# Kernel optimization log

Measured on AMD Instinct MI355X. Metric: run time of the kernel, lower is better.

Reference implementation:

```python
import jax, jax.numpy as jnp
from jax import lax
import numpy as np

R_ICO = 6          # resolution exponent r
CIN, COUT = 64, 64
RIN, ROUT = 6, 6
CHARTS = 5
H, W = 2 ** R_ICO, 2 ** (R_ICO + 1)
BATCH = 4


def _build_reorder_idx(r, R):
    H_, W_ = 2 ** r, 2 ** (r + 1)
    p = 2 ** r
    idx_in = np.arange(R * 5 * H_ * W_, dtype=np.int64).reshape(R, 5, H_, W_)
    out = np.zeros((R, 5, H_ + 2, W_ + 2), dtype=np.int64)
    out[..., 1:-1, 1:-1] = idx_in
    out[..., 0, 1:p + 1] = np.roll(idx_in, 1, -3)[..., -1, p:]
    out[..., 0, p + 1:-1] = np.roll(np.roll(idx_in, 1, -3), -1, -4)[..., :, -1][..., ::-1]
    out[..., -1, 2:p + 2] = np.roll(np.roll(idx_in, -1, -3), -1, -4)[..., :, 0][..., ::-1]
    out[..., -1, p + 1:-1] = np.roll(idx_in, -1, -3)[..., 0, 0:p]
    out[..., 1:-1, 0] = np.roll(np.roll(idx_in, 1, -3), 1, -4)[..., -1, 0:p][..., ::-1]
    out[..., 2:, -1] = np.roll(np.roll(idx_in, -1, -3), 1, -4)[..., 0, p:][..., ::-1]
    return out


_REORDER = jnp.asarray(_build_reorder_idx(R_ICO, RIN))

# 'baseline' hexagonal kernel index table (idx_k2 == idx_k for baseline)
_IDX_K = np.array([
    [5, 4, -1, 6, 0, 3, -1, 1, 2],
    [4, 3, -1, 5, 0, 2, -1, 6, 1],
    [3, 2, -1, 4, 0, 1, -1, 5, 6],
    [2, 1, -1, 3, 0, 6, -1, 4, 5],
    [1, 6, -1, 2, 0, 5, -1, 3, 4],
    [6, 5, -1, 1, 0, 4, -1, 2, 3]], dtype=np.int64) % 7
# per-output-rotation roll of the Rin axis: idx_r = arange(Rin) rolled i times
_RIN_MAP = np.stack([np.roll(np.arange(RIN), i) for i in range(ROUT)])  # (Rout, Rin)
_MASK3 = np.ones((3, 3), dtype=np.float32)
_MASK3[0, 2] = 0.0  # ret[..., 0, 2] = 0
_MASK3[2, 0] = 0.0  # ret[..., 2, 0] = 0

# CleanVertices: zero the two pole vertices of each chart
_VMASK = np.ones((H, W), dtype=np.float32)
_VMASK[0, -1] = 0.0
_VMASK[-1, 0] = 0.0


def _expand_kernel(weight):
    # weight: (Cout, Cin, Rin, 7)
    # K[co, ci, i, rj, k] = weight[co, ci, rin_map[i, rj], idx_k[i, k]]
    K = weight[:, :, _RIN_MAP[:, :, None], _IDX_K[:, None, :]]  # (Cout, Cin, Rout, Rin, 9)
    K = K.transpose(0, 2, 1, 3, 4).reshape(COUT, ROUT, CIN, RIN, 3, 3)
    K = K * _MASK3  # zero hex-grid corner taps
    # kernel_type='baseline' => idx_k2 == idx_k, so 0.5*K + 0.5*K2 == K
    return K.reshape(COUT * ROUT, CIN * RIN, 3, 3)


def setup_inputs() -> dict:
    key = jax.random.key(0)
    kx, kw = jax.random.split(key)
    s = float(np.sqrt(2.0 / (3 * 3 * CIN * RIN)))
    x = jax.random.normal(kx, (BATCH, CIN, RIN, CHARTS, H, W), dtype=jnp.float32)
    weight = s * jax.random.normal(kw, (COUT, CIN, RIN, 7), dtype=jnp.float32)
    bias = jnp.zeros((COUT,), dtype=jnp.float32)
    return {"x": x, "weight": weight, "bias": bias}


def reference(x, weight, bias):
    B = x.shape[0]
    # CleanVertices on input (inside PadIco.process_vertices)
    x = x * _VMASK
    # icosahedral gather padding: [B, C, R, 5, H, W] -> [B, C, R, 5, H+2, W+2]
    xf = x.reshape(B, CIN, -1)
    xp = jnp.take(xf, _REORDER, axis=-1)
    # fold (C R) -> channels and (charts, H+2) -> height
    ximg = xp.reshape(B, CIN * RIN, CHARTS * (H + 2), W + 2)
    kernel = _expand_kernel(weight)
    y = lax.conv_general_dilated(ximg, kernel, (1, 1), ((1, 1), (1, 1)),
                                 dimension_numbers=('NCHW', 'OIHW', 'NCHW'))
    y = y + jnp.repeat(bias, ROUT)[None, :, None, None]
    y = y.reshape(B, COUT, ROUT, CHARTS, H + 2, W + 2)[..., 1:-1, 1:-1]
    # CleanVertices on output
    return y * _VMASK
```

## Files before the change

kernel.cpp:

```cpp
#include <hip/hip_runtime.h>
#include <hip/hip_bf16.h>

#define BB    4
#define CIN_  64
#define RIN_  6
#define CH_   5
#define HH    64
#define WW_   128
#define KD    384
#define MD    384
#define PH    66
#define PW    130
#define PSZ   (PH*PW)

#define NTAP 7
#define WEXP2_ELEMS (NTAP*MD*KD)
#define WEXP2_BYTES (WEXP2_ELEMS*2)

#define NB_INTERIOR 7680
#define NB_BORDER   380
#define NB_WEXP     4032
#define NB_PREP     (NB_INTERIOR + NB_BORDER + NB_WEXP)

typedef __hip_bfloat16 bf16;
typedef __attribute__((ext_vector_type(8))) short bf16x8;
typedef __attribute__((ext_vector_type(4))) float f32x4;

__device__ const int TMAP[NTAP] = {0,1,3,4,5,7,8};
__device__ const int IDXK[6][9] = {
    {5,4,6,6,0,3,6,1,2},
    {4,3,6,5,0,2,6,6,1},
    {3,2,6,4,0,1,6,5,6},
    {2,1,6,3,0,6,6,4,5},
    {1,6,6,2,0,5,6,3,4},
    {6,5,6,1,0,4,6,2,3},
};

__global__ __launch_bounds__(256) void prep_kernel(const float* __restrict__ x,
                                                   const float* __restrict__ w,
                                                   bf16* __restrict__ P,
                                                   bf16* __restrict__ W2) {
    const int blk = blockIdx.x;
    const int tid = threadIdx.x;

    if (blk < NB_INTERIOR) {
        int bid  = blk;
        int kblk = bid % 3;
        int xh   = (bid / 3) & 1;
        int y    = (bid / 6) % 64;
        int bc   = bid / 384;
        int c = bc % 5, b = bc / 5;

        int lane = tid & 63;
        int wv   = tid >> 6;
        int k0   = kblk * 128 + wv * 32;
        int sx   = xh * 64 + lane;
        int xx   = sx + 1;

        bool mask0 = (y == 0 && sx == 127) || (y == 63 && sx == 0);

        const float* src = x + ((((size_t)(b * 384 + k0) * 5 + c) * 64 + y) * 128 + sx);
        unsigned int hbuf[16];
        #pragma unroll
        for (int kk = 0; kk < 32; kk += 2) {
            float v1 = src[(size_t)kk * 40960];
            float v2 = src[(size_t)(kk + 1) * 40960];
            if (mask0) { v1 = 0.f; v2 = 0.f; }
            bf16 h1 = __float2bfloat16(v1);
            bf16 h2 = __float2bfloat16(v2);
            hbuf[kk >> 1] = ((unsigned int)*(unsigned short*)&h2 << 16) |
                            (unsigned int)*(unsigned short*)&h1;
        }
        bf16* dst = P + (((size_t)(b * 5 + c) * PH + (y + 1)) * PW + xx) * KD + k0;
        uint4* d4 = (uint4*)dst;
        #pragma unroll
        for (int q = 0; q < 4; ++q)
            d4[q] = make_uint4(hbuf[4*q], hbuf[4*q+1], hbuf[4*q+2], hbuf[4*q+3]);
        return;
    }

    if (blk < NB_INTERIOR + NB_BORDER) {
        int bidB = blk - NB_INTERIOR;
        int bc   = bidB / 19;
        int idx  = (bidB % 19) * 256 + tid;
        if (idx >= 12 * 388) return;
        int c = bc % 5, b = bc / 5;
        int chunk = idx / 388;
        int p     = idx % 388;

        int yy, xx;
        if (p < 130)      { yy = 0;  xx = p; }
        else if (p < 260) { yy = 65; xx = p - 130; }
        else if (p < 324) { yy = 1 + (p - 260); xx = 0; }
        else              { yy = 1 + (p - 324); xx = 129; }

        int dr = 0, sc = c, sy = 0, sx = 0;
        bool zi = false;
        if (xx == 129) {
            if (yy >= 2) { dr = 5; sc = (c + 1) % 5; sy = 0; sx = 129 - yy; }
            else zi = true;
        } else if (yy == 0) {
            if (xx >= 1 && xx <= 64)        { dr = 0; sc = (c + 4) % 5; sy = 63; sx = 63 + xx; }
            else if (xx >= 65 && xx <= 128) { dr = 1; sc = (c + 4) % 5; sy = 128 - xx; sx = 127; }
            else zi = true;
        } else if (yy == 65) {
            if (xx >= 65 && xx <= 128)      { dr = 0; sc = (c + 1) % 5; sy = 0; sx = xx - 65; }
            else if (xx >= 2 && xx <= 64)   { dr = 1; sc = (c + 1) % 5; sy = 65 - xx; sx = 0; }
            else zi = true;
        } else {
            dr = 5; sc = (c + 4) % 5; sy = 63; sx = 64 - yy;
        }
        if (zi) { dr = 0; sc = 0; sy = 0; sx = 0; }
        bool kill = !zi && ((sy == 0 && sx == 127) || (sy == 63 && sx == 0));

        const size_t SBASE = ((size_t)(b * 1920 + sc)) * 8192 + sy * 128 + sx;
        const int k0 = chunk * 32;

        unsigned int hb[16];
        #pragma unroll
        for (int kk = 0; kk < 32; ++kk) {
            int k  = k0 + kk;
            int ci = k / 6;
            int r  = k - 6 * ci;
            int sr = zi ? 0 : ((r + dr >= 6) ? r + dr - 6 : r + dr);
            float v = x[SBASE + (size_t)(ci * 6 + sr) * 40960];
            if (kill) v = 0.f;
            bf16 h = __float2bfloat16(v);
            unsigned int hu = (unsigned int)*(unsigned short*)&h;
            if (kk & 1) hb[kk >> 1] |= hu << 16;
            else        hb[kk >> 1]  = hu;
        }
        bf16* dst = P + (((size_t)(b * 5 + c) * PH + yy) * PW + xx) * KD + k0;
        uint4* d4 = (uint4*)dst;
        #pragma unroll
        for (int q = 0; q < 4; ++q)
            d4[q] = make_uint4(hb[4*q], hb[4*q+1], hb[4*q+2], hb[4*q+3]);
        return;
    }

    {
        int e = (blk - NB_INTERIOR - NB_BORDER) * 256 + tid;
        if (e >= WEXP2_ELEMS) return;
        int k  = e % KD;
        int m  = (e / KD) % MD;
        int tt = e / (KD * MD);
        int t  = TMAP[tt];
        int co = m / 6, ro = m % 6, ci = k / 6, ri = k % 6;
        int rw = (ri - ro + 6) % 6;
        int s  = IDXK[ro][t];
        W2[e] = __float2bfloat16(w[((co * CIN_ + ci) * RIN_ + rw) * 7 + s]);
    }
}

#define DYP 0x2950
#define DXP 0x2644

#define GLD(g, l) __builtin_amdgcn_global_load_lds( \
    (const __attribute__((address_space(1))) void*)(g), \
    (__attribute__((address_space(3))) void*)(l), 16, 0, 0)
#define MFMA_(a, b, c) __builtin_amdgcn_mfma_f32_16x16x32_bf16((a), (b), (c), 0, 0, 0)

__global__ __launch_bounds__(256, 2) void conv_mfma4(
        const bf16* __restrict__ P, const bf16* __restrict__ W2,
        const float* __restrict__ bias, float* __restrict__ out) {
    __shared__ __align__(16) bf16 As[3][4096];
    __shared__ __align__(16) bf16 Bs[3][8192];

    const int bid = blockIdx.x;
    const int w   = (bid & 7) * 240 + (bid >> 3);
    const int mblk  = w % 3;
    const int ntile = (w / 3) % 32;
    const int bc    = w / 96;
    const int c = bc % 5, b = bc / 5;
    const int y0 = ntile * 2;

    const int tid  = threadIdx.x;
    const int lane = tid & 63;
    const int wv   = tid >> 6;
    const int lm   = lane & 15, lg = lane >> 4;

    const bf16* Pslice = P + (size_t)(b * 5 + c) * PSZ * KD;

    int oA[8], oB[4];
    #pragma unroll
    for (int i = 0; i < 8; ++i) {
        int mm = i * 16 + lm;
        oA[i] = (mm * 4 + (lg ^ ((mm >> 1) & 3))) * 16;
    }
    #pragma unroll
    for (int j = 0; j < 4; ++j) {
        int nn = wv * 64 + j * 16 + lm;
        oB[j] = (nn * 4 + (lg ^ ((nn >> 1) & 3))) * 16;
    }
    const char* Ab = (const char*)&As[0][0];
    const char* Bb = (const char*)&Bs[0][0];

    const bf16* gA[2];
    #pragma unroll
    for (int q = 0; q < 2; ++q) {
        int s = wv * 128 + q * 64 + lane;
        int row = s >> 2, j = s & 3;
        gA[q] = W2 + (size_t)(mblk * 128 + row) * KD + ((j ^ ((row >> 1) & 3)) << 3);
    }
    const bf16* gB[4];
    #pragma unroll
    for (int q = 0; q < 4; ++q) {
        int s = wv * 256 + q * 64 + lane;
        int col = s >> 2, j = s & 3;
        int ncol = (col & 127) + (col >> 7) * PW;
        gB[q] = Pslice + (size_t)ncol * KD + ((j ^ ((col >> 1) & 3)) << 3);
    }

    f32x4 acc[8][4] = {};

    #pragma unroll
    for (int t = 0; t < 2; ++t) {
        size_t offA = (size_t)t * 32;
        size_t offB = (size_t)y0 * PW * KD + t * 32;
        GLD(gA[0] + offA, &As[t][(wv * 128) * 8]);
        GLD(gA[1] + offA, &As[t][(wv * 128 + 64) * 8]);
        #pragma unroll
        for (int q = 0; q < 4; ++q)
            GLD(gB[q] + offB, &Bs[t][(wv * 256 + q * 64) * 8]);
    }
    asm volatile("s_waitcnt vmcnt(6)" ::: "memory");
    __builtin_amdgcn_s_barrier();

    #pragma unroll 1
    for (int tt = 0; tt < 7; ++tt) {
        #pragma unroll
        for (int kc = 0; kc < 12; ++kc) {
            const int rb   = kc % 3;
            const int sb   = (kc + 2) % 3;
            const int skc  = (kc + 2) % 12;
            const int stt  = tt + (kc + 2) / 12;
            const bool dostage = (stt < 7);
            const bool drain   = (tt == 6 && kc >= 10);

            bf16x8 a0 = *(const bf16x8*)(Ab + rb * 8192 + oA[0]);
            bf16x8 a1 = *(const bf16x8*)(Ab + rb * 8192 + oA[1]);
            bf16x8 a2 = *(const bf16x8*)(Ab + rb * 8192 + oA[2]);
            bf16x8 a3 = *(const bf16x8*)(Ab + rb * 8192 + oA[3]);
            bf16x8 a4 = *(const bf16x8*)(Ab + rb * 8192 + oA[4]);
            bf16x8 a5 = *(const bf16x8*)(Ab + rb * 8192 + oA[5]);
            bf16x8 a6 = *(const bf16x8*)(Ab + rb * 8192 + oA[6]);
            bf16x8 a7 = *(const bf16x8*)(Ab + rb * 8192 + oA[7]);
            bf16x8 b0 = *(const bf16x8*)(Bb + rb * 16384 + oB[0]);
            bf16x8 b1 = *(const bf16x8*)(Bb + rb * 16384 + oB[1]);
            bf16x8 b2 = *(const bf16x8*)(Bb + rb * 16384 + oB[2]);
            bf16x8 b3 = *(const bf16x8*)(Bb + rb * 16384 + oB[3]);

            if (dostage) {
                const int dy = (DYP >> (2 * stt)) & 3;
                const int dx = (DXP >> (2 * stt)) & 3;
                size_t offA = (size_t)stt * (MD * KD) + skc * 32;
                size_t offB = ((size_t)(y0 + dy) * PW + dx) * KD + skc * 32;
                GLD(gA[0] + offA, &As[sb][(wv * 128) * 8]);
                GLD(gA[1] + offA, &As[sb][(wv * 128 + 64) * 8]);
                GLD(gB[0] + offB, &Bs[sb][(wv * 256) * 8]);
                GLD(gB[1] + offB, &Bs[sb][(wv * 256 + 64) * 8]);
                GLD(gB[2] + offB, &Bs[sb][(wv * 256 + 128) * 8]);
                GLD(gB[3] + offB, &Bs[sb][(wv * 256 + 192) * 8]);
            }

            __builtin_amdgcn_s_setprio(1);
            acc[0][0] = MFMA_(a0, b0, acc[0][0]);
            acc[1][0] = MFMA_(a1, b0, acc[1][0]);
            acc[2][0] = MFMA_(a2, b0, acc[2][0]);
            acc[3][0] = MFMA_(a3, b0, acc[3][0]);
            acc[4][0] = MFMA_(a4, b0, acc[4][0]);
            acc[5][0] = MFMA_(a5, b0, acc[5][0]);
            acc[6][0] = MFMA_(a6, b0, acc[6][0]);
            acc[7][0] = MFMA_(a7, b0, acc[7][0]);
            acc[0][1] = MFMA_(a0, b1, acc[0][1]);
            acc[1][1] = MFMA_(a1, b1, acc[1][1]);
            acc[2][1] = MFMA_(a2, b1, acc[2][1]);
            acc[3][1] = MFMA_(a3, b1, acc[3][1]);
            acc[4][1] = MFMA_(a4, b1, acc[4][1]);
            acc[5][1] = MFMA_(a5, b1, acc[5][1]);
            acc[6][1] = MFMA_(a6, b1, acc[6][1]);
            acc[7][1] = MFMA_(a7, b1, acc[7][1]);
            acc[0][2] = MFMA_(a0, b2, acc[0][2]);
            acc[1][2] = MFMA_(a1, b2, acc[1][2]);
            acc[2][2] = MFMA_(a2, b2, acc[2][2]);
            acc[3][2] = MFMA_(a3, b2, acc[3][2]);
            acc[4][2] = MFMA_(a4, b2, acc[4][2]);
            acc[5][2] = MFMA_(a5, b2, acc[5][2]);
            acc[6][2] = MFMA_(a6, b2, acc[6][2]);
            acc[7][2] = MFMA_(a7, b2, acc[7][2]);
            acc[0][3] = MFMA_(a0, b3, acc[0][3]);
            acc[1][3] = MFMA_(a1, b3, acc[1][3]);
            acc[2][3] = MFMA_(a2, b3, acc[2][3]);
            acc[3][3] = MFMA_(a3, b3, acc[3][3]);
            acc[4][3] = MFMA_(a4, b3, acc[4][3]);
            acc[5][3] = MFMA_(a5, b3, acc[5][3]);
            acc[6][3] = MFMA_(a6, b3, acc[6][3]);
            acc[7][3] = MFMA_(a7, b3, acc[7][3]);
            __builtin_amdgcn_s_setprio(0);

            if (drain) {
                asm volatile("s_waitcnt vmcnt(0)" ::: "memory");
            } else {
                asm volatile("s_waitcnt vmcnt(6)" ::: "memory");
            }
            __builtin_amdgcn_s_barrier();
        }
    }

    const int m0 = mblk * 128;
    const int yq = y0 + (wv >> 1);
    const int xb = (wv & 1) * 64;
    #pragma unroll
    for (int i = 0; i < 8; ++i) {
        #pragma unroll
        for (int r = 0; r < 4; ++r) {
            int m = m0 + i * 16 + lg * 4 + r;
            float bv = bias[m / 6];
            #pragma unroll
            for (int j = 0; j < 4; ++j) {
                int xq = xb + j * 16 + lm;
                float v = acc[i][j][r] + bv;
                if ((yq == 0 && xq == 127) || (yq == 63 && xq == 0)) v = 0.f;
                out[((size_t)(b * MD + m) * CH_ + c) * (HH * WW_) + yq * WW_ + xq] = v;
            }
        }
    }
}

extern "C" void kernel_launch(void* const* d_in, const int* in_sizes, int n_in,
                              void* d_out, int out_size, void* d_ws, size_t ws_size,
                              hipStream_t stream) {
    const float* x    = (const float*)d_in[0];
    const float* w    = (const float*)d_in[1];
    const float* bias = (const float*)d_in[2];
    float* out        = (float*)d_out;

    bf16* W2 = (bf16*)d_ws;
    bf16* P  = (bf16*)((char*)d_ws + WEXP2_BYTES);

    prep_kernel<<<NB_PREP, 256, 0, stream>>>(x, w, P, W2);

    conv_mfma4<<<1920, 256, 0, stream>>>(P, W2, bias, out);
}
```

Before: 480.2 us.

## Replace shared LDS pipeline with barrier-free per-wave private double buffering

```diff
diff --git a/kernel.cpp b/kernel.cpp
--- a/kernel.cpp
+++ b/kernel.cpp
@@ -160,11 +160,10 @@
     (__attribute__((address_space(3))) void*)(l), 16, 0, 0)
 #define MFMA_(a, b, c) __builtin_amdgcn_mfma_f32_16x16x32_bf16((a), (b), (c), 0, 0, 0)
 
-__global__ __launch_bounds__(256, 2) void conv_mfma4(
+__global__ __launch_bounds__(512, 2) void conv_free(
         const bf16* __restrict__ P, const bf16* __restrict__ W2,
         const float* __restrict__ bias, float* __restrict__ out) {
-    __shared__ __align__(16) bf16 As[3][4096];
-    __shared__ __align__(16) bf16 Bs[3][8192];
+    __shared__ __align__(16) bf16 Ss[65536];
 
     const int bid = blockIdx.x;
     const int w   = (bid & 7) * 240 + (bid >> 3);
@@ -177,151 +176,115 @@
     const int tid  = threadIdx.x;
     const int lane = tid & 63;
     const int wv   = tid >> 6;
+    const int wm   = wv >> 2;
+    const int wn   = wv & 3;
     const int lm   = lane & 15, lg = lane >> 4;
 
+    const int mA0 = mblk * 128 + wm * 64;
+    const int ry  = y0 + (wn >> 1);
+    const int cx  = (wn & 1) * 64;
+
     const bf16* Pslice = P + (size_t)(b * 5 + c) * PSZ * KD;
 
-    int oA[8], oB[4];
-    #pragma unroll
-    for (int i = 0; i < 8; ++i) {
-        int mm = i * 16 + lm;
-        oA[i] = (mm * 4 + (lg ^ ((mm >> 1) & 3))) * 16;
-    }
-    #pragma unroll
-    for (int j = 0; j < 4; ++j) {
-        int nn = wv * 64 + j * 16 + lm;
-        oB[j] = (nn * 4 + (lg ^ ((nn >> 1) & 3))) * 16;
-    }
-    const char* Ab = (const char*)&As[0][0];
-    const char* Bb = (const char*)&Bs[0][0];
-
-    const bf16* gA[2];
-    #pragma unroll
-    for (int q = 0; q < 2; ++q) {
-        int s = wv * 128 + q * 64 + lane;
-        int row = s >> 2, j = s & 3;
-        gA[q] = W2 + (size_t)(mblk * 128 + row) * KD + ((j ^ ((row >> 1) & 3)) << 3);
-    }
+    const bf16* gA[4];
     const bf16* gB[4];
     #pragma unroll
     for (int q = 0; q < 4; ++q) {
-        int s = wv * 256 + q * 64 + lane;
-        int col = s >> 2, j = s & 3;
-        int ncol = (col & 127) + (col >> 7) * PW;
-        gB[q] = Pslice + (size_t)ncol * KD + ((j ^ ((col >> 1) & 3)) << 3);
-    }
-
-    f32x4 acc[8][4] = {};
-
+        int s = q * 64 + lane;
+        int row = s >> 2, kg = s & 3;
+        gA[q] = W2 + (size_t)(mA0 + row) * KD + ((kg ^ ((row >> 1) & 3)) << 3);
+        gB[q] = Pslice + (size_t)row * KD + ((kg ^ ((row >> 1) & 3)) << 3);
+    }
+
+    const int wvByte = wv * 16384;
+    int oA[4], oB[4];
     #pragma unroll
-    for (int t = 0; t < 2; ++t) {
-        size_t offA = (size_t)t * 32;
-        size_t offB = (size_t)y0 * PW * KD + t * 32;
-        GLD(gA[0] + offA, &As[t][(wv * 128) * 8]);
-        GLD(gA[1] + offA, &As[t][(wv * 128 + 64) * 8]);
+    for (int i = 0; i < 4; ++i) {
+        int mm = i * 16 + lm;
+        oA[i] = (mm * 4 + (lg ^ ((mm >> 1) & 3))) * 16;
+        oB[i] = (mm * 4 + (lg ^ ((mm >> 1) & 3))) * 16 + 4096;
+    }
+    const char* Sb = (const char*)&Ss[0];
+
+
+    f32x4 acc[4][4] = {};
+
+    {
+        size_t offB = ((size_t)ry * PW + cx) * KD;
         #pragma unroll
         for (int q = 0; q < 4; ++q)
-            GLD(gB[q] + offB, &Bs[t][(wv * 256 + q * 64) * 8]);
-    }
-    asm volatile("s_waitcnt vmcnt(6)" ::: "memory");
-    __builtin_amdgcn_s_barrier();
+            GLD(gA[q], (char*)&Ss[0] + wvByte + q * 1024);
+        #pragma unroll
+        for (int q = 0; q < 4; ++q)
+            GLD(gB[q] + offB, (char*)&Ss[0] + wvByte + 4096 + q * 1024);
+    }
+    asm volatile("s_waitcnt vmcnt(0)" ::: "memory");
 
     #pragma unroll 1
-    for (int tt = 0; tt < 7; ++tt) {
-        #pragma unroll
-        for (int kc = 0; kc < 12; ++kc) {
-            const int rb   = kc % 3;
-            const int sb   = (kc + 2) % 3;
-            const int skc  = (kc + 2) % 12;
-            const int stt  = tt + (kc + 2) / 12;
-            const bool dostage = (stt < 7);
-            const bool drain   = (tt == 6 && kc >= 10);
-
-            bf16x8 a0 = *(const bf16x8*)(Ab + rb * 8192 + oA[0]);
-            bf16x8 a1 = *(const bf16x8*)(Ab + rb * 8192 + oA[1]);
-            bf16x8 a2 = *(const bf16x8*)(Ab + rb * 8192 + oA[2]);
-            bf16x8 a3 = *(const bf16x8*)(Ab + rb * 8192 + oA[3]);
-            bf16x8 a4 = *(const bf16x8*)(Ab + rb * 8192 + oA[4]);
-            bf16x8 a5 = *(const bf16x8*)(Ab + rb * 8192 + oA[5]);
-            bf16x8 a6 = *(const bf16x8*)(Ab + rb * 8192 + oA[6]);
-            bf16x8 a7 = *(const bf16x8*)(Ab + rb * 8192 + oA[7]);
-            bf16x8 b0 = *(const bf16x8*)(Bb + rb * 16384 + oB[0]);
-            bf16x8 b1 = *(const bf16x8*)(Bb + rb * 16384 + oB[1]);
-            bf16x8 b2 = *(const bf16x8*)(Bb + rb * 16384 + oB[2]);
-            bf16x8 b3 = *(const bf16x8*)(Bb + rb * 16384 + oB[3]);
-
-            if (dostage) {
-                const int dy = (DYP >> (2 * stt)) & 3;
-                const int dx = (DXP >> (2 * stt)) & 3;
-                size_t offA = (size_t)stt * (MD * KD) + skc * 32;
-                size_t offB = ((size_t)(y0 + dy) * PW + dx) * KD + skc * 32;
-                GLD(gA[0] + offA, &As[sb][(wv * 128) * 8]);
-                GLD(gA[1] + offA, &As[sb][(wv * 128 + 64) * 8]);
-                GLD(gB[0] + offB, &Bs[sb][(wv * 256) * 8]);
-                GLD(gB[1] + offB, &Bs[sb][(wv * 256 + 64) * 8]);
-                GLD(gB[2] + offB, &Bs[sb][(wv * 256 + 128) * 8]);
-                GLD(gB[3] + offB, &Bs[sb][(wv * 256 + 192) * 8]);
-            }
-
-            __builtin_amdgcn_s_setprio(1);
-            acc[0][0] = MFMA_(a0, b0, acc[0][0]);
-            acc[1][0] = MFMA_(a1, b0, acc[1][0]);
-            acc[2][0] = MFMA_(a2, b0, acc[2][0]);
-            acc[3][0] = MFMA_(a3, b0, acc[3][0]);
-            acc[4][0] = MFMA_(a4, b0, acc[4][0]);
-            acc[5][0] = MFMA_(a5, b0, acc[5][0]);
-            acc[6][0] = MFMA_(a6, b0, acc[6][0]);
-            acc[7][0] = MFMA_(a7, b0, acc[7][0]);
-            acc[0][1] = MFMA_(a0, b1, acc[0][1]);
-            acc[1][1] = MFMA_(a1, b1, acc[1][1]);
-            acc[2][1] = MFMA_(a2, b1, acc[2][1]);
-            acc[3][1] = MFMA_(a3, b1, acc[3][1]);
-            acc[4][1] = MFMA_(a4, b1, acc[4][1]);
-            acc[5][1] = MFMA_(a5, b1, acc[5][1]);
-            acc[6][1] = MFMA_(a6, b1, acc[6][1]);
-            acc[7][1] = MFMA_(a7, b1, acc[7][1]);
-            acc[0][2] = MFMA_(a0, b2, acc[0][2]);
-            acc[1][2] = MFMA_(a1, b2, acc[1][2]);
-            acc[2][2] = MFMA_(a2, b2, acc[2][2]);
-            acc[3][2] = MFMA_(a3, b2, acc[3][2]);
-            acc[4][2] = MFMA_(a4, b2, acc[4][2]);
-            acc[5][2] = MFMA_(a5, b2, acc[5][2]);
-            acc[6][2] = MFMA_(a6, b2, acc[6][2]);
-            acc[7][2] = MFMA_(a7, b2, acc[7][2]);
-            acc[0][3] = MFMA_(a0, b3, acc[0][3]);
-            acc[1][3] = MFMA_(a1, b3, acc[1][3]);
-            acc[2][3] = MFMA_(a2, b3, acc[2][3]);
-            acc[3][3] = MFMA_(a3, b3, acc[3][3]);
-            acc[4][3] = MFMA_(a4, b3, acc[4][3]);
-            acc[5][3] = MFMA_(a5, b3, acc[5][3]);
-            acc[6][3] = MFMA_(a6, b3, acc[6][3]);
-            acc[7][3] = MFMA_(a7, b3, acc[7][3]);
-            __builtin_amdgcn_s_setprio(0);
-
-            if (drain) {
-                asm volatile("s_waitcnt vmcnt(0)" ::: "memory");
-            } else {
-                asm volatile("s_waitcnt vmcnt(6)" ::: "memory");
-            }
-            __builtin_amdgcn_s_barrier();
-        }
-    }
-
-    const int m0 = mblk * 128;
-    const int yq = y0 + (wv >> 1);
-    const int xb = (wv & 1) * 64;
+    for (int ch = 0; ch < 84; ++ch) {
+        const int bufB = (ch & 1) * 8192;
+
+        if (ch < 83) {
+            int nch = ch + 1;
+            int stt = nch / 12;
+            int skc = nch - stt * 12;
+            int dy  = (DYP >> (2 * stt)) & 3;
+            int dx  = (DXP >> (2 * stt)) & 3;
+            size_t offA = (size_t)stt * (MD * KD) + skc * 32;
+            size_t offB = ((size_t)(ry + dy) * PW + dx + cx) * KD + skc * 32;
+            const int nb = ((ch + 1) & 1) * 8192;
+            #pragma unroll
+            for (int q = 0; q < 4; ++q)
+                GLD(gA[q] + offA, (char*)&Ss[0] + wvByte + nb + q * 1024);
+            #pragma unroll
+            for (int q = 0; q < 4; ++q)
+                GLD(gB[q] + offB, (char*)&Ss[0] + wvByte + nb + 4096 + q * 1024);
+        }
+
+        bf16x8 a0 = *(const bf16x8*)(Sb + wvByte + bufB + oA[0]);
+        bf16x8 a1 = *(const bf16x8*)(Sb + wvByte + bufB + oA[1]);
+        bf16x8 a2 = *(const bf16x8*)(Sb + wvByte + bufB + oA[2]);
+        bf16x8 a3 = *(const bf16x8*)(Sb + wvByte + bufB + oA[3]);
+        bf16x8 b0 = *(const bf16x8*)(Sb + wvByte + bufB + oB[0]);
+        bf16x8 b1 = *(const bf16x8*)(Sb + wvByte + bufB + oB[1]);
+        bf16x8 b2 = *(const bf16x8*)(Sb + wvByte + bufB + oB[2]);
+        bf16x8 b3 = *(const bf16x8*)(Sb + wvByte + bufB + oB[3]);
+
+        __builtin_amdgcn_s_setprio(1);
+        acc[0][0] = MFMA_(a0, b0, acc[0][0]);
+        acc[1][0] = MFMA_(a1, b0, acc[1][0]);
+        acc[2][0] = MFMA_(a2, b0, acc[2][0]);
+        acc[3][0] = MFMA_(a3, b0, acc[3][0]);
+        acc[0][1] = MFMA_(a0, b1, acc[0][1]);
+        acc[1][1] = MFMA_(a1, b1, acc[1][1]);
+        acc[2][1] = MFMA_(a2, b1, acc[2][1]);
+        acc[3][1] = MFMA_(a3, b1, acc[3][1]);
+        acc[0][2] = MFMA_(a0, b2, acc[0][2]);
+        acc[1][2] = MFMA_(a1, b2, acc[1][2]);
+        acc[2][2] = MFMA_(a2, b2, acc[2][2]);
+        acc[3][2] = MFMA_(a3, b2, acc[3][2]);
+        acc[0][3] = MFMA_(a0, b3, acc[0][3]);
+        acc[1][3] = MFMA_(a1, b3, acc[1][3]);
+        acc[2][3] = MFMA_(a2, b3, acc[2][3]);
+        acc[3][3] = MFMA_(a3, b3, acc[3][3]);
+        __builtin_amdgcn_s_setprio(0);
+
+        if (ch < 83)
+            asm volatile("s_waitcnt vmcnt(0)" ::: "memory");
+    }
+
     #pragma unroll
-    for (int i = 0; i < 8; ++i) {
+    for (int i = 0; i < 4; ++i) {
         #pragma unroll
         for (int r = 0; r < 4; ++r) {
-            int m = m0 + i * 16 + lg * 4 + r;
+            int m = mA0 + i * 16 + lg * 4 + r;
             float bv = bias[m / 6];
             #pragma unroll
             for (int j = 0; j < 4; ++j) {
-                int xq = xb + j * 16 + lm;
+                int xq = cx + j * 16 + lm;
                 float v = acc[i][j][r] + bv;
-                if ((yq == 0 && xq == 127) || (yq == 63 && xq == 0)) v = 0.f;
-                out[((size_t)(b * MD + m) * CH_ + c) * (HH * WW_) + yq * WW_ + xq] = v;
+                if ((ry == 0 && xq == 127) || (ry == 63 && xq == 0)) v = 0.f;
+                out[((size_t)(b * MD + m) * CH_ + c) * (HH * WW_) + ry * WW_ + xq] = v;
             }
         }
     }
@@ -340,5 +303,5 @@
 
     prep_kernel<<<NB_PREP, 256, 0, stream>>>(x, w, P, W2);
 
-    conv_mfma4<<<1920, 256, 0, stream>>>(P, W2, bias, out);
+    conv_free<<<1920, 512, 0, stream>>>(P, W2, bias, out);
 }
```

Result: slower. 669.5 us (median of 2 runs) (+39.4%).
